# Kernel tuning notes

Measured on AMD Instinct MI355X. Metric: run time of the kernel, lower is better.

## Reference

```python
import jax, jax.numpy as jnp
import numpy as np

NUM_BINS = 256
WS = 5          # ssim_window_size
SIGMA = 1.5
LEVELS = 5
MS_WEIGHTS = jnp.asarray(np.array([0.0448, 0.2856, 0.3001, 0.2363, 0.1333], dtype=np.float32))


def _gauss_window():
    x = np.arange(WS) - WS // 2
    g = np.exp(-(x.astype(np.float64) ** 2) / (2.0 * SIGMA ** 2))
    g = g / g.sum()
    return jnp.asarray(np.outer(g, g), dtype=jnp.float32)  # (WS, WS)


def _conv_same(x, w):
    # x: (H, W), w: (WS, WS); 'SAME' pad == torch padding=WS//2 for odd WS
    return jax.lax.conv_general_dilated(x[None, None], w[None, None], (1, 1), 'SAME')[0, 0]


def _rgb_to_lab(img):
    # img: (3, H, W) in [0,1] -> normalized LAB (3, H, W)  (CURL ImageProcessing.rgb_to_lab)
    H, W = img.shape[1], img.shape[2]
    x = jnp.transpose(img, (2, 1, 0)).reshape(-1, 3)  # (W*H, 3)
    lin = jnp.where(x <= 0.04045, x / 12.92,
                    ((jnp.maximum(x, 1e-4) + 0.055) / 1.055) ** 2.4)
    rgb2xyz = jnp.array([[0.412453, 0.212671, 0.019334],
                         [0.357580, 0.715160, 0.119193],
                         [0.180423, 0.072169, 0.950227]], dtype=img.dtype)
    xyz = lin @ rgb2xyz
    xyz = xyz * jnp.array([1.0 / 0.950456, 1.0, 1.0 / 1.088754], dtype=img.dtype)
    eps = 6.0 / 29.0
    f = jnp.where(xyz <= eps ** 3,
                  xyz / (3.0 * eps ** 2) + 4.0 / 29.0,
                  jnp.maximum(xyz, 1e-4) ** (1.0 / 3.0))
    f2lab = jnp.array([[0.0, 500.0, 0.0],
                       [116.0, -500.0, 200.0],
                       [0.0, 0.0, -200.0]], dtype=img.dtype)
    lab = f @ f2lab + jnp.array([-16.0, 0.0, 0.0], dtype=img.dtype)
    lab = jnp.transpose(lab.reshape(W, H, 3), (2, 1, 0))  # (3, H, W)
    return jnp.stack([lab[0] / 100.0,
                      (lab[1] / 110.0 + 1.0) / 2.0,
                      (lab[2] / 110.0 + 1.0) / 2.0])


def _histogram(img):
    # img: (3, H, W) in [0,1] -> per-channel 256-bin count histogram (3, NUM_BINS)
    idx = jnp.clip(jnp.floor(img * NUM_BINS).astype(jnp.int32), 0, NUM_BINS - 1)
    per_ch = lambda ix: jnp.zeros((NUM_BINS,), jnp.float32).at[ix.reshape(-1)].add(1.0)
    return jax.vmap(per_ch)(idx)


def _ssim(i1, i2, w):
    # i1, i2: (H, W) single-channel images
    mu1 = _conv_same(i1, w)
    mu2 = _conv_same(i2, w)
    s1 = _conv_same(i1 * i1, w) - mu1 * mu1
    s2 = _conv_same(i2 * i2, w) - mu2 * mu2
    s12 = _conv_same(i1 * i2, w) - mu1 * mu2
    C1, C2 = 0.01 ** 2, 0.03 ** 2
    ssim_map = ((2.0 * mu1 * mu2 + C1) * (2.0 * s12 + C2)) / \
               ((mu1 * mu1 + mu2 * mu2 + C1) * (s1 + s2 + C2))
    cs = jnp.mean((2.0 * s12 + C2) / (s1 + s2 + C2))
    return ssim_map.mean(), cs


def _avg_pool2(x):
    H, W = x.shape
    return x.reshape(H // 2, 2, W // 2, 2).mean(axis=(1, 3))


def _msssim(i1, i2, w):
    mssim, mcs = [], []
    for _ in range(LEVELS):
        s, cs = _ssim(i1, i2, w)
        mssim.append(s)
        mcs.append(cs)
        i1 = _avg_pool2(i1)
        i2 = _avg_pool2(i2)
    mssim = (jnp.stack(mssim) + 1.0) / 2.0
    mcs = (jnp.stack(mcs) + 1.0) / 2.0
    return jnp.prod(mcs[:LEVELS - 1] ** MS_WEIGHTS[:LEVELS - 1]) * mssim[LEVELS - 1] ** MS_WEIGHTS[LEVELS - 1]


def _forward(input_image_batch, predicted_img_batch, target_img_batch):
    pred_lab = jnp.clip(jax.vmap(_rgb_to_lab)(predicted_img_batch), 0.0, 1.0)
    tgt_lab = jnp.clip(jax.vmap(_rgb_to_lab)(target_img_batch), 0.0, 1.0)

    # histogram loss: original loop does h_i = (h_{i-1} + l1_i + 1) / 2; closed form below
    hp = jax.vmap(_histogram)(pred_lab)   # (B, 3, NUM_BINS)
    ht = jax.vmap(_histogram)(tgt_lab)
    l1_hist = jnp.mean(jnp.abs(hp - ht), axis=(1, 2))  # (B,)
    n = l1_hist.shape[0]
    wgt = 2.0 ** (jnp.arange(n, dtype=jnp.float32) - n)  # 2^{-(n-i)}
    hist_loss = jnp.sum(wgt * (l1_hist + 1.0))

    # MS-SSIM on L channel, per image (is_identity=True -> no variational_prediction)
    window = _gauss_window()
    ms = jax.vmap(lambda a, b: _msssim(a, b, window))(pred_lab[:, 0], tgt_lab[:, 0])
    ssim_loss = jnp.mean(1.0 - ms)

    lab_l1 = jnp.mean(jnp.abs(pred_lab - tgt_lab))  # mean of per-image means (same-size imgs)

    H, W = input_image_batch.shape[2], input_image_batch.shape[3]
    scaler = H * W / 20.0
    hist_loss = hist_loss / n / scaler
    lab_loss = lab_l1 + hist_loss
    return lab_loss.reshape(1, 1), ssim_loss.reshape(1, 1)


def setup_inputs():
    key = jax.random.key(0)
    k1, k2, k3 = jax.random.split(key, 3)
    B, C, H, W = 8, 3, 512, 512
    return {
        'input_image_batch': jax.random.uniform(k1, (B, C, H, W), jnp.float32),
        'predicted_img_batch': jax.random.uniform(k2, (B, C, H, W), jnp.float32),
        'target_img_batch': jax.random.uniform(k3, (B, C, H, W), jnp.float32),
        'is_identity': 1,
    }


def reference(input_image_batch, predicted_img_batch, target_img_batch, is_identity):
    return _forward(input_image_batch, predicted_img_batch, target_img_batch)
```

## Files before the change

kernel.cpp:

```cpp
#include <hip/hip_runtime.h>
#include <math.h>

#define B 8
#define IMH 512
#define IMW 512
#define HW (IMH*IMW)
#define NBINS 256

#define PYR_PER_IMG (65536 + 16384 + 4096 + 1024)
#define PYR_OFF_L1 0
#define PYR_OFF_L2 65536
#define PYR_OFF_L3 81920
#define PYR_OFF_L4 86016

#define OFF_PPYR 0
#define OFF_TPYR (B*PYR_PER_IMG)
#define OFF_HISTPART (2*B*PYR_PER_IMG)
#define OFF_LABPART  (OFF_HISTPART + B*256*768)
#define OFF_CSP      (OFF_LABPART + B*256)
#define OFF_LVLS     (OFF_CSP + B*256)
#define OFF_LVLC     (OFF_LVLS + B*85)
#define OFF_HISTL1   (OFF_LVLC + B*85)

typedef float f2 __attribute__((ext_vector_type(2)));

__device__ __forceinline__ f2 mkf2(float a, float b) { f2 r; r.x = a; r.y = b; return r; }
__device__ __forceinline__ f2 shfl_down_f2(f2 v, int d) {
    return mkf2(__shfl_down(v.x, d, 64), __shfl_down(v.y, d, 64));
}
__device__ __forceinline__ f2 shfl_f2(f2 v, int src) {
    return mkf2(__shfl(v.x, src, 64), __shfl(v.y, src, 64));
}
__device__ __forceinline__ f2 clamp01_f2(f2 a) {
    a.x = fminf(fmaxf(a.x, 0.0f), 1.0f);
    a.y = fminf(fmaxf(a.y, 0.0f), 1.0f);
    return a;
}

__device__ __forceinline__ float fastpow(float x, float y) {
    return __builtin_amdgcn_exp2f(y * __builtin_amdgcn_logf(x));
}

__device__ __forceinline__ void rgb2lab_pk(f2 r, f2 g, f2 b, f2 lab[3]) {
    f2 v[3] = {r, g, b};
    f2 lin[3];
    #pragma unroll
    for (int c = 0; c < 3; ++c) {
        f2 x = v[c];
        float hx = fastpow((fmaxf(x.x, 1e-4f) + 0.055f) * (float)(1.0/1.055), 2.4f);
        float hy = fastpow((fmaxf(x.y, 1e-4f) + 0.055f) * (float)(1.0/1.055), 2.4f);
        lin[c].x = (x.x <= 0.04045f) ? x.x * (float)(1.0/12.92) : hx;
        lin[c].y = (x.y <= 0.04045f) ? x.y * (float)(1.0/12.92) : hy;
    }
    f2 X = 0.412453f*lin[0] + 0.357580f*lin[1] + 0.180423f*lin[2];
    f2 Y = 0.212671f*lin[0] + 0.715160f*lin[1] + 0.072169f*lin[2];
    f2 Z = 0.019334f*lin[0] + 0.119193f*lin[1] + 0.950227f*lin[2];
    X = X * (float)(1.0/0.950456);
    Z = Z * (float)(1.0/1.088754);
    const float eps3   = (float)((6.0/29.0)*(6.0/29.0)*(6.0/29.0));
    const float rd3e2  = (float)(1.0/(3.0*(6.0/29.0)*(6.0/29.0)));
    const float c429   = (float)(4.0/29.0);
    f2 xyz[3] = {X, Y, Z};
    f2 f[3];
    #pragma unroll
    for (int c = 0; c < 3; ++c) {
        float ax = xyz[c].x, ay = xyz[c].y;
        f[c].x = (ax <= eps3) ? (ax * rd3e2 + c429) : fastpow(fmaxf(ax, 1e-4f), (float)(1.0/3.0));
        f[c].y = (ay <= eps3) ? (ay * rd3e2 + c429) : fastpow(fmaxf(ay, 1e-4f), (float)(1.0/3.0));
    }
    f2 L  = 116.0f*f[1] - 16.0f;
    f2 A  = 500.0f*f[0] - 500.0f*f[1];
    f2 Bc = 200.0f*f[1] - 200.0f*f[2];
    lab[0] = L * 0.01f;
    lab[1] = (A * (float)(1.0/110.0) + 1.0f) * 0.5f;
    lab[2] = (Bc * (float)(1.0/110.0) + 1.0f) * 0.5f;
}

#define TST 37

template<bool WANT_S>
__device__ __forceinline__ void conv_ssim(const f2* tile, int t, float& ssum, float& csum) {
    double gd[5]; double gs = 0.0;
    #pragma unroll
    for (int i = 0; i < 5; ++i) { gd[i] = exp(-(double)((i-2)*(i-2)) / 4.5); gs += gd[i]; }
    float gw[5];
    #pragma unroll
    for (int i = 0; i < 5; ++i) gw[i] = (float)(gd[i] / gs);

    int lx = t & 31;
    int yg = t >> 5;

    f2 rA[8], rB[8];
    float r12[8];
    #pragma unroll
    for (int k = 0; k < 8; ++k) {
        int row = yg * 4 + k;
        const f2* p = &tile[row * TST + lx];
        f2 sA = {0.f, 0.f}, sB = {0.f, 0.f};
        float s12 = 0.f;
        #pragma unroll
        for (int dx = 0; dx < 5; ++dx) {
            f2 av = p[dx];
            float wv = gw[dx];
            sA += wv * av;
            f2 sq = av * av;
            sB += wv * sq;
            s12 = fmaf(wv, av.x * av.y, s12);
        }
        rA[k] = sA; rB[k] = sB; r12[k] = s12;
    }

    const float C1 = (float)(0.01 * 0.01);
    const float C2 = (float)(0.03 * 0.03);
    if constexpr (WANT_S) ssum = 0.f;
    csum = 0.f;
    #pragma unroll
    for (int j = 0; j < 4; ++j) {
        f2 mA = {0.f, 0.f}, mB = {0.f, 0.f};
        float m12 = 0.f;
        #pragma unroll
        for (int k = 0; k < 5; ++k) {
            float wv = gw[k];
            mA += wv * rA[j + k];
            mB += wv * rB[j + k];
            m12 = fmaf(wv, r12[j + k], m12);
        }
        float m1 = mA.x, m2 = mA.y;
        float v1  = mB.x - m1 * m1;
        float v2  = mB.y - m2 * m2;
        float v12 = m12 - m1 * m2;
        float n12 = 2.0f * v12 + C2;
        float rd2 = __builtin_amdgcn_rcpf(v1 + v2 + C2);
        csum = fmaf(n12, rd2, csum);
        if constexpr (WANT_S) {
            float rd1 = __builtin_amdgcn_rcpf(m1*m1 + m2*m2 + C1);
            ssum += (2.0f*m1*m2 + C1) * n12 * rd1 * rd2;
        }
    }
}

__device__ __forceinline__ void halo_coords(int h, int& hr, int& hc) {
    if (h < 72)       { hr = h / 36;            hc = h % 36; }
    else if (h < 144) { int u = h - 72;  hr = 34 + u / 36; hc = u % 36; }
    else              { int u = h - 144; hr = 2 + (u >> 2); int q = u & 3; hc = (q < 2) ? q : 32 + q; }
}

__global__ void lab_ssim0_kernel(const float* __restrict__ pred,
                                 const float* __restrict__ tgt,
                                 unsigned* __restrict__ histPart,
                                 float* __restrict__ labPart,
                                 float* __restrict__ csPart,
                                 float* __restrict__ ppyr,
                                 float* __restrict__ tpyr) {
    __shared__ f2 ls[36 * TST];
    __shared__ unsigned lhist[6 * NBINS];
    __shared__ f2 s1[16 * 16];
    __shared__ float red12[12];

    int t  = threadIdx.x;
    int b  = blockIdx.y;
    int bx = blockIdx.x;

    for (int i = t; i < 6 * NBINS; i += 256) lhist[i] = 0;
    __syncthreads();

    int tile = ((bx & 7) << 5) | (bx >> 3);
    int tx0 = (tile & 15) << 5;
    int ty0 = (tile >> 4) << 5;
    int r   = t >> 3;
    int c4  = (t & 7) << 2;
    int gy  = ty0 + r;

    const float* pimg = pred + (size_t)b * 3 * HW;
    const float* timg = tgt  + (size_t)b * 3 * HW;
    size_t ibase = (size_t)gy * IMW + tx0 + c4;

    float prA[4], pgA[4], pbA[4], trA[4], tgA[4], tbA[4];
    *(float4*)&prA[0] = *(const float4*)(pimg + ibase);
    *(float4*)&pgA[0] = *(const float4*)(pimg + ibase + HW);
    *(float4*)&pbA[0] = *(const float4*)(pimg + ibase + 2*HW);
    *(float4*)&trA[0] = *(const float4*)(timg + ibase);
    *(float4*)&tgA[0] = *(const float4*)(timg + ibase + HW);
    *(float4*)&tbA[0] = *(const float4*)(timg + ibase + 2*HW);

    int hr0, hc0;
    halo_coords(t, hr0, hc0);
    int hy0 = ty0 - 2 + hr0;
    int hx0 = tx0 - 2 + hc0;
    bool hv0 = ((unsigned)hy0 < 512u) && ((unsigned)hx0 < 512u);
    size_t ho = hv0 ? ((size_t)hy0 * IMW + hx0) : 0;
    float h_pr = pimg[ho], h_pg = pimg[ho + HW], h_pb = pimg[ho + 2*HW];
    float h_tr = timg[ho], h_tg = timg[ho + HW], h_tb = timg[ho + 2*HW];

    float l1 = 0.0f;
    f2 pL[4];
    #pragma unroll
    for (int k = 0; k < 4; ++k) {
        f2 lab[3];
        rgb2lab_pk(mkf2(prA[k], trA[k]), mkf2(pgA[k], tgA[k]), mkf2(pbA[k], tbA[k]), lab);
        #pragma unroll
        for (int c = 0; c < 3; ++c) {
            f2 lc = clamp01_f2(lab[c]);
            l1 += fabsf(lc.x - lc.y);
            int ip = min(max((int)floorf(lc.x * (float)NBINS), 0), NBINS - 1);
            int it = min(max((int)floorf(lc.y * (float)NBINS), 0), NBINS - 1);
            atomicAdd(&lhist[c * NBINS + ip], 1u);
            atomicAdd(&lhist[(3 + c) * NBINS + it], 1u);
            if (c == 0) pL[k] = lc;
        }
        ls[(r + 2) * TST + (c4 + 2 + k)] = pL[k];
    }

    {
        f2 lab[3];
        rgb2lab_pk(mkf2(h_pr, h_tr), mkf2(h_pg, h_tg), mkf2(h_pb, h_tb), lab);
        f2 Lv = hv0 ? clamp01_f2(lab[0]) : mkf2(0.f, 0.f);
        ls[hr0 * TST + hc0] = Lv;
    }
    if (t < 16) {
        int hr, hc;
        halo_coords(256 + t, hr, hc);
        int hy = ty0 - 2 + hr;
        int hx = tx0 - 2 + hc;
        f2 Lv = {0.f, 0.f};
        if ((unsigned)hy < 512u && (unsigned)hx < 512u) {
            size_t o = (size_t)hy * IMW + hx;
            f2 lab[3];
            rgb2lab_pk(mkf2(pimg[o], timg[o]),
                       mkf2(pimg[o + HW], timg[o + HW]),
                       mkf2(pimg[o + 2*HW], timg[o + 2*HW]), lab);
            Lv = clamp01_f2(lab[0]);
        }
        ls[hr * TST + hc] = Lv;
    }
    __syncthreads();

    unsigned* hp = histPart + ((size_t)b * 256 + bx) * 768;
    for (int i = t; i < 768; i += 256)
        hp[i] = (lhist[2*i] & 0xFFFFu) | (lhist[2*i + 1] << 16);

    float* pyrP = ppyr + (size_t)b * PYR_PER_IMG;
    float* pyrT = tpyr + (size_t)b * PYR_PER_IMG;
    f2 ph0 = pL[0] + pL[1], ph1 = pL[2] + pL[3];
    f2 ph0b = shfl_down_f2(ph0, 8);
    f2 ph1b = shfl_down_f2(ph1, 8);
    if ((t & 8) == 0) {
        int y1 = r >> 1;
        int x1 = (t & 7) << 1;
        f2 v0 = 0.25f * (ph0 + ph0b);
        f2 v1 = 0.25f * (ph1 + ph1b);
        s1[y1 * 16 + x1]     = v0;
        s1[y1 * 16 + x1 + 1] = v1;
        int g1 = ((ty0 >> 1) + y1) * 256 + (tx0 >> 1) + x1;
        *(float2*)&pyrP[PYR_OFF_L1 + g1] = make_float2(v0.x, v1.x);
        *(float2*)&pyrT[PYR_OFF_L1 + g1] = make_float2(v0.y, v1.y);
    }
    __syncthreads();

    float sdummy, csum;
    conv_ssim<false>(ls, t, sdummy, csum);

    if (t < 64) {
        int y2 = t >> 3, x2 = t & 7;
        const f2* s = &s1[(2*y2) * 16 + 2*x2];
        f2 v2 = 0.25f * (s[0] + s[1] + s[16] + s[17]);
        pyrP[PYR_OFF_L2 + ((ty0 >> 2) + y2) * 128 + (tx0 >> 2) + x2] = v2.x;
        pyrT[PYR_OFF_L2 + ((ty0 >> 2) + y2) * 128 + (tx0 >> 2) + x2] = v2.y;

        int y3 = (t >> 2) & 3, x3 = t & 3;
        f2 v3 = 0.25f * (shfl_f2(v2, (2*y3)*8 + 2*x3)     + shfl_f2(v2, (2*y3)*8 + 2*x3 + 1) +
                         shfl_f2(v2, (2*y3+1)*8 + 2*x3)   + shfl_f2(v2, (2*y3+1)*8 + 2*x3 + 1));
        if (t < 16) {
            pyrP[PYR_OFF_L3 + ((ty0 >> 3) + y3) * 64 + (tx0 >> 3) + x3] = v3.x;
            pyrT[PYR_OFF_L3 + ((ty0 >> 3) + y3) * 64 + (tx0 >> 3) + x3] = v3.y;
        }
        int y4 = (t >> 1) & 1, x4 = t & 1;
        f2 v4 = 0.25f * (shfl_f2(v3, (2*y4)*4 + 2*x4)     + shfl_f2(v3, (2*y4)*4 + 2*x4 + 1) +
                         shfl_f2(v3, (2*y4+1)*4 + 2*x4)   + shfl_f2(v3, (2*y4+1)*4 + 2*x4 + 1));
        if (t < 4) {
            pyrP[PYR_OFF_L4 + ((ty0 >> 4) + y4) * 32 + (tx0 >> 4) + x4] = v4.x;
            pyrT[PYR_OFF_L4 + ((ty0 >> 4) + y4) * 32 + (tx0 >> 4) + x4] = v4.y;
        }
    }

    int lane = t & 63;
    int wid  = t >> 6;
    #pragma unroll
    for (int o = 32; o >= 1; o >>= 1) {
        l1   += __shfl_down(l1, o, 64);
        csum += __shfl_down(csum, o, 64);
    }
    if (lane == 0) {
        red12[wid * 2 + 0] = l1;
        red12[wid * 2 + 1] = csum;
    }
    __syncthreads();
    if (t < 4) {
        float a0 = red12[t * 2 + 0];
        float a2 = red12[t * 2 + 1];
        #pragma unroll
        for (int o = 2; o >= 1; o >>= 1) {
            a0 += __shfl_down(a0, o, 64);
            a2 += __shfl_down(a2, o, 64);
        }
        if (t == 0) {
            labPart[b * 256 + bx] = a0;
            csPart[b * 256 + bx]  = a2;
        }
    }
}

__global__ void tail_kernel(const float* __restrict__ ppyr,
                            const float* __restrict__ tpyr,
                            const unsigned* __restrict__ histPart,
                            float* __restrict__ lvlS,
                            float* __restrict__ lvlC,
                            float* __restrict__ histL1p) {
    __shared__ f2 tls[36 * TST];
    __shared__ float red12[12];
    __shared__ int dLo[256];
    __shared__ int dHi[256];
    int t = threadIdx.x;
    int bx = blockIdx.x;

    if (bx < 48) {
        int b  = bx / 6;
        int w  = (bx % 6) * 64 + (t & 63);
        int ck = t >> 6;
        const unsigned* p = histPart + (size_t)b * 256 * 768 + (size_t)(ck * 64) * 768;
        unsigned sPlo = 0, sPhi = 0, sTlo = 0, sThi = 0;
        #pragma unroll 8
        for (int i = 0; i < 64; ++i) {
            unsigned wP = p[(size_t)i * 768 + w];
            unsigned wT = p[(size_t)i * 768 + 384 + w];
            sPlo += wP & 0xFFFFu;  sPhi += wP >> 16;
            sTlo += wT & 0xFFFFu;  sThi += wT >> 16;
        }
        dLo[t] = (int)sPlo - (int)sTlo;
        dHi[t] = (int)sPhi - (int)sThi;
        __syncthreads();
        if (t < 64) {
            int lo = dLo[t] + dLo[t + 64] + dLo[t + 128] + dLo[t + 192];
            int hi = dHi[t] + dHi[t + 64] + dHi[t + 128] + dHi[t + 192];
            float val = fabsf((float)lo) + fabsf((float)hi);
            #pragma unroll
            for (int o = 32; o >= 1; o >>= 1) val += __shfl_down(val, o, 64);
            if (t == 0) histL1p[bx] = val;
        }
    } else {
        int cb = bx - 48;
        int b = cb / 85;
        int sub = cb - b * 85;
        int lvl, pblk;
        if (sub < 64)      { lvl = 1; pblk = sub; }
        else if (sub < 80) { lvl = 2; pblk = sub - 64; }
        else if (sub < 84) { lvl = 3; pblk = sub - 80; }
        else               { lvl = 4; pblk = 0; }

        const int offs[5] = {0, PYR_OFF_L1, PYR_OFF_L2, PYR_OFF_L3, PYR_OFF_L4};
        int w = 512 >> lvl;
        const float* i1 = ppyr + (size_t)b * PYR_PER_IMG + offs[lvl];
        const float* i2 = tpyr + (size_t)b * PYR_PER_IMG + offs[lvl];

        int tprShift = 4 - lvl;
        int ty0 = (pblk >> tprShift) << 5;
        int tx0 = (pblk & ((1 << tprShift) - 1)) << 5;

        for (int i = t; i < 36 * 36; i += 256) {
            int r = i / 36, c = i % 36;
            int gy = ty0 - 2 + r;
            int gx = tx0 - 2 + c;
            bool ok = ((unsigned)gy < (unsigned)w) && ((unsigned)gx < (unsigned)w);
            int gi = gy * w + gx;
            tls[r * TST + c] = ok ? mkf2(i1[gi], i2[gi]) : mkf2(0.f, 0.f);
        }
        __syncthreads();

        float ssum, csum;
        conv_ssim<true>(tls, t, ssum, csum);

        int lane = t & 63;
        int wid  = t >> 6;
        #pragma unroll
        for (int o = 32; o >= 1; o >>= 1) {
            ssum += __shfl_down(ssum, o, 64);
            csum += __shfl_down(csum, o, 64);
        }
        if (lane == 0) {
            red12[wid * 2 + 0] = ssum;
            red12[wid * 2 + 1] = csum;
        }
        __syncthreads();
        if (t < 4) {
            float a1 = red12[t * 2 + 0];
            float a2 = red12[t * 2 + 1];
            #pragma unroll
            for (int o = 2; o >= 1; o >>= 1) {
                a1 += __shfl_down(a1, o, 64);
                a2 += __shfl_down(a2, o, 64);
            }
            if (t == 0) {
                lvlS[cb] = a1;
                lvlC[cb] = a2;
            }
        }
    }
}

__global__ void final_kernel(const float* __restrict__ labPart,
                             const float* __restrict__ csPart,
                             const float* __restrict__ lvlS,
                             const float* __restrict__ lvlC,
                             const float* __restrict__ histL1p,
                             float* __restrict__ out) {
    __shared__ double sh[48];
    __shared__ double wred[4];
    int t = threadIdx.x;

    {
        int b = t >> 5, k = t & 31;
        double s = 0.0;
        #pragma unroll
        for (int j = 0; j < 8; ++j) s += (double)csPart[b * 256 + k + 32 * j];
        #pragma unroll
        for (int o = 16; o >= 1; o >>= 1) s += __shfl_down(s, o, 32);
        if (k == 0) sh[b] = s;
    }
    {
        double s = 0.0;
        #pragma unroll
        for (int j = 0; j < 8; ++j) s += (double)labPart[t + 256 * j];
        #pragma unroll
        for (int o = 32; o >= 1; o >>= 1) s += __shfl_down(s, o, 64);
        if ((t & 63) == 0) wred[t >> 6] = s;
    }
    if (t < 32) {
        int b = t >> 2, q = t & 3;
        const int lo[4] = {0, 64, 80, 84};
        const int hi[4] = {64, 80, 84, 85};
        const float* src = (q == 3) ? lvlS : lvlC;
        double s = 0.0;
        for (int i = lo[q]; i < hi[q]; ++i) s += (double)src[b * 85 + i];
        sh[8 + q * 8 + b] = s;
    }
    if (t < 8) {
        double s = 0.0;
        #pragma unroll
        for (int j = 0; j < 6; ++j) s += (double)histL1p[t * 6 + j];
        sh[40 + t] = s;
    }
    __syncthreads();

    if (t < 8) {
        const float msw[5]  = {0.0448f, 0.2856f, 0.3001f, 0.2363f, 0.1333f};
        const float npix[5] = {(float)HW, (float)(HW/4), (float)(HW/16),
                               (float)(HW/64), (float)(HW/256)};
        int b = t;
        float l1 = (float)(sh[40 + b] / (double)(3 * NBINS));
        float wgt = __builtin_amdgcn_exp2f((float)(b - B));
        float histc = wgt * (l1 + 1.0f);
        float ms = 1.0f;
        float cs0 = (float)(sh[b] / (double)npix[0]);
        ms *= fastpow((cs0 + 1.0f) * 0.5f, msw[0]);
        #pragma unroll
        for (int l = 1; l <= 3; ++l) {
            float cs = (float)(sh[l * 8 + b] / (double)npix[l]);
            ms *= fastpow((cs + 1.0f) * 0.5f, msw[l]);
        }
        float sm = (float)(sh[32 + b] / (double)npix[4]);
        ms *= fastpow((sm + 1.0f) * 0.5f, msw[4]);
        float lossc = 1.0f - ms;
        #pragma unroll
        for (int o = 4; o >= 1; o >>= 1) {
            histc += __shfl_down(histc, o, 64);
            lossc += __shfl_down(lossc, o, 64);
        }
        if (t == 0) {
            double labSum = wred[0] + wred[1] + wred[2] + wred[3];
            float scaler = (float)HW / 20.0f;
            float hist_loss = histc / (float)B / scaler;
            float lab_l1 = (float)(sh[40] * 0.0 + labSum / (double)((size_t)B * 3 * HW));
            out[0] = lab_l1 + hist_loss;
            out[1] = lossc / (float)B;
        }
    }
}

extern "C" void kernel_launch(void* const* d_in, const int* in_sizes, int n_in,
                              void* d_out, int out_size, void* d_ws, size_t ws_size,
                              hipStream_t stream) {
    const float* pred = (const float*)d_in[1];
    const float* tgt  = (const float*)d_in[2];
    float* ws_f = (float*)d_ws;

    float* ppyr     = ws_f + OFF_PPYR;
    float* tpyr     = ws_f + OFF_TPYR;
    unsigned* histPart = (unsigned*)(ws_f + OFF_HISTPART);
    float* labPart  = ws_f + OFF_LABPART;
    float* csPart   = ws_f + OFF_CSP;
    float* lvlS     = ws_f + OFF_LVLS;
    float* lvlC     = ws_f + OFF_LVLC;
    float* histL1p  = ws_f + OFF_HISTL1;
    float* out = (float*)d_out;


    lab_ssim0_kernel<<<dim3(256, B), 256, 0, stream>>>(pred, tgt, histPart, labPart,
                                                       csPart, ppyr, tpyr);

    tail_kernel<<<728, 256, 0, stream>>>(ppyr, tpyr, histPart, lvlS, lvlC, histL1p);

    final_kernel<<<1, 256, 0, stream>>>(labPart, csPart, lvlS, lvlC, histL1p, out);
}
```

Before: 129.9 us.

## Widen first-stage tiles to 64x32 with separable SSIM convolution

Each first-stage block now covers a 64x32 tile instead of 32x32, halving the block count and the number of per-block partial histograms the tail kernel must reduce. The 5x5 SSIM window is computed separably: horizontal sums go into a rolling register buffer, then a vertical pass. The pyramid downsampling is remapped to the wider tile, and one barrier is removed. This lowers halo overhead and partial-histogram traffic, at the cost of more registers per thread and fewer blocks to spread across the GPU.

```diff
diff --git a/kernel.cpp b/kernel.cpp
--- a/kernel.cpp
+++ b/kernel.cpp
@@ -13,12 +13,14 @@
 #define PYR_OFF_L3 81920
 #define PYR_OFF_L4 86016
 
+#define NTILE 128
+
 #define OFF_PPYR 0
 #define OFF_TPYR (B*PYR_PER_IMG)
 #define OFF_HISTPART (2*B*PYR_PER_IMG)
-#define OFF_LABPART  (OFF_HISTPART + B*256*768)
-#define OFF_CSP      (OFF_LABPART + B*256)
-#define OFF_LVLS     (OFF_CSP + B*256)
+#define OFF_LABPART  (OFF_HISTPART + B*NTILE*768)
+#define OFF_CSP      (OFF_LABPART + B*NTILE)
+#define OFF_LVLS     (OFF_CSP + B*NTILE)
 #define OFF_LVLC     (OFF_LVLS + B*85)
 #define OFF_HISTL1   (OFF_LVLC + B*85)
 
@@ -77,6 +79,7 @@
 }
 
 #define TST 37
+#define WT  69
 
 template<bool WANT_S>
 __device__ __forceinline__ void conv_ssim(const f2* tile, int t, float& ssum, float& csum) {
@@ -139,10 +142,59 @@
     }
 }
 
-__device__ __forceinline__ void halo_coords(int h, int& hr, int& hc) {
-    if (h < 72)       { hr = h / 36;            hc = h % 36; }
-    else if (h < 144) { int u = h - 72;  hr = 34 + u / 36; hc = u % 36; }
-    else              { int u = h - 144; hr = 2 + (u >> 2); int q = u & 3; hc = (q < 2) ? q : 32 + q; }
+__device__ __forceinline__ void hsum5(const f2* p, const float* gw, f2& A, f2& Bq, float& s12) {
+    A = mkf2(0.f, 0.f); Bq = mkf2(0.f, 0.f); s12 = 0.f;
+    #pragma unroll
+    for (int dx = 0; dx < 5; ++dx) {
+        f2 av = p[dx];
+        float wv = gw[dx];
+        A += wv * av;
+        Bq += wv * (av * av);
+        s12 = fmaf(wv, av.x * av.y, s12);
+    }
+}
+
+__device__ __forceinline__ float conv_cs_wide(const f2* tile, int t) {
+    double gd[5]; double gs = 0.0;
+    #pragma unroll
+    for (int i = 0; i < 5; ++i) { gd[i] = exp(-(double)((i-2)*(i-2)) / 4.5); gs += gd[i]; }
+    float gw[5];
+    #pragma unroll
+    for (int i = 0; i < 5; ++i) gw[i] = (float)(gd[i] / gs);
+
+    int x  = t & 63;
+    int R0 = (t >> 6) * 8;
+    const f2* base = tile + x;
+
+    f2 hA[8], hB[8]; float h12[8];
+    #pragma unroll
+    for (int k = 0; k < 8; ++k)
+        hsum5(base + (R0 + k) * WT, gw, hA[k], hB[k], h12[k]);
+
+    const float C2 = (float)(0.03 * 0.03);
+    float csum = 0.f;
+    auto emit = [&](int i0, int i1, int i2, int i3, int i4) {
+        f2 mA = gw[0]*hA[i0] + gw[1]*hA[i1] + gw[2]*hA[i2] + gw[3]*hA[i3] + gw[4]*hA[i4];
+        f2 mB = gw[0]*hB[i0] + gw[1]*hB[i1] + gw[2]*hB[i2] + gw[3]*hB[i3] + gw[4]*hB[i4];
+        float m12 = gw[0]*h12[i0] + gw[1]*h12[i1] + gw[2]*h12[i2] + gw[3]*h12[i3] + gw[4]*h12[i4];
+        float m1 = mA.x, m2 = mA.y;
+        float v1  = mB.x - m1 * m1;
+        float v2v = mB.y - m2 * m2;
+        float v12 = m12 - m1 * m2;
+        csum = fmaf(2.0f * v12 + C2, __builtin_amdgcn_rcpf(v1 + v2v + C2), csum);
+    };
+    emit(0,1,2,3,4); emit(1,2,3,4,5); emit(2,3,4,5,6); emit(3,4,5,6,7);
+    hsum5(base + (R0 +  8) * WT, gw, hA[0], hB[0], h12[0]); emit(4,5,6,7,0);
+    hsum5(base + (R0 +  9) * WT, gw, hA[1], hB[1], h12[1]); emit(5,6,7,0,1);
+    hsum5(base + (R0 + 10) * WT, gw, hA[2], hB[2], h12[2]); emit(6,7,0,1,2);
+    hsum5(base + (R0 + 11) * WT, gw, hA[3], hB[3], h12[3]); emit(7,0,1,2,3);
+    return csum;
+}
+
+__device__ __forceinline__ void halo68(int h, int& hr, int& hc) {
+    if (h < 136)      { hr = h / 68;            hc = h % 68; }
+    else if (h < 272) { int u = h - 136; hr = 34 + u / 68; hc = u % 68; }
+    else              { int u = h - 272; hr = 2 + (u >> 2); int q = u & 3; hc = (q < 2) ? q : q + 64; }
 }
 
 __global__ void lab_ssim0_kernel(const float* __restrict__ pred,
@@ -152,9 +204,9 @@
                                  float* __restrict__ csPart,
                                  float* __restrict__ ppyr,
                                  float* __restrict__ tpyr) {
-    __shared__ f2 ls[36 * TST];
+    __shared__ f2 ls[36 * WT];
     __shared__ unsigned lhist[6 * NBINS];
-    __shared__ f2 s1[16 * 16];
+    __shared__ f2 s1[16 * 32];
     __shared__ float red12[12];
 
     int t  = threadIdx.x;
@@ -164,40 +216,52 @@
     for (int i = t; i < 6 * NBINS; i += 256) lhist[i] = 0;
     __syncthreads();
 
-    int tile = ((bx & 7) << 5) | (bx >> 3);
-    int tx0 = (tile & 15) << 5;
-    int ty0 = (tile >> 4) << 5;
+    int tile = ((bx & 7) << 4) | (bx >> 3);
+    int tx0 = (tile & 7) << 6;
+    int ty0 = (tile >> 3) << 5;
     int r   = t >> 3;
-    int c4  = (t & 7) << 2;
+    int c8  = (t & 7) << 3;
     int gy  = ty0 + r;
 
     const float* pimg = pred + (size_t)b * 3 * HW;
     const float* timg = tgt  + (size_t)b * 3 * HW;
-    size_t ibase = (size_t)gy * IMW + tx0 + c4;
-
-    float prA[4], pgA[4], pbA[4], trA[4], tgA[4], tbA[4];
-    *(float4*)&prA[0] = *(const float4*)(pimg + ibase);
-    *(float4*)&pgA[0] = *(const float4*)(pimg + ibase + HW);
-    *(float4*)&pbA[0] = *(const float4*)(pimg + ibase + 2*HW);
-    *(float4*)&trA[0] = *(const float4*)(timg + ibase);
-    *(float4*)&tgA[0] = *(const float4*)(timg + ibase + HW);
-    *(float4*)&tbA[0] = *(const float4*)(timg + ibase + 2*HW);
-
-    int hr0, hc0;
-    halo_coords(t, hr0, hc0);
-    int hy0 = ty0 - 2 + hr0;
-    int hx0 = tx0 - 2 + hc0;
-    bool hv0 = ((unsigned)hy0 < 512u) && ((unsigned)hx0 < 512u);
-    size_t ho = hv0 ? ((size_t)hy0 * IMW + hx0) : 0;
-    float h_pr = pimg[ho], h_pg = pimg[ho + HW], h_pb = pimg[ho + 2*HW];
-    float h_tr = timg[ho], h_tg = timg[ho + HW], h_tb = timg[ho + 2*HW];
+    size_t ibase = (size_t)gy * IMW + tx0 + c8;
+
+    float pr[8], pg[8], pb[8], tr[8], tg[8], tb[8];
+    *(float4*)&pr[0] = *(const float4*)(pimg + ibase);
+    *(float4*)&pr[4] = *(const float4*)(pimg + ibase + 4);
+    *(float4*)&pg[0] = *(const float4*)(pimg + ibase + HW);
+    *(float4*)&pg[4] = *(const float4*)(pimg + ibase + HW + 4);
+    *(float4*)&pb[0] = *(const float4*)(pimg + ibase + 2*HW);
+    *(float4*)&pb[4] = *(const float4*)(pimg + ibase + 2*HW + 4);
+    *(float4*)&tr[0] = *(const float4*)(timg + ibase);
+    *(float4*)&tr[4] = *(const float4*)(timg + ibase + 4);
+    *(float4*)&tg[0] = *(const float4*)(timg + ibase + HW);
+    *(float4*)&tg[4] = *(const float4*)(timg + ibase + HW + 4);
+    *(float4*)&tb[0] = *(const float4*)(timg + ibase + 2*HW);
+    *(float4*)&tb[4] = *(const float4*)(timg + ibase + 2*HW + 4);
+
+    int hrA, hcA; halo68(t, hrA, hcA);
+    int hyA = ty0 - 2 + hrA, hxA = tx0 - 2 + hcA;
+    bool hvA = ((unsigned)hyA < 512u) && ((unsigned)hxA < 512u);
+    size_t hoA = hvA ? ((size_t)hyA * IMW + hxA) : 0;
+    float aPr = pimg[hoA], aPg = pimg[hoA + HW], aPb = pimg[hoA + 2*HW];
+    float aTr = timg[hoA], aTg = timg[hoA + HW], aTb = timg[hoA + 2*HW];
+
+    bool hasB = t < 144;
+    int hrB, hcB; halo68(hasB ? (256 + t) : 0, hrB, hcB);
+    int hyB = ty0 - 2 + hrB, hxB = tx0 - 2 + hcB;
+    bool hvB = hasB && ((unsigned)hyB < 512u) && ((unsigned)hxB < 512u);
+    size_t hoB = hvB ? ((size_t)hyB * IMW + hxB) : 0;
+    float bPr = pimg[hoB], bPg = pimg[hoB + HW], bPb = pimg[hoB + 2*HW];
+    float bTr = timg[hoB], bTg = timg[hoB + HW], bTb = timg[hoB + 2*HW];
 
     float l1 = 0.0f;
-    f2 pL[4];
-    #pragma unroll
-    for (int k = 0; k < 4; ++k) {
+    f2 pL[8];
+    #pragma unroll
+    for (int k = 0; k < 8; ++k) {
         f2 lab[3];
-        rgb2lab_pk(mkf2(prA[k], trA[k]), mkf2(pgA[k], tgA[k]), mkf2(pbA[k], tbA[k]), lab);
+        rgb2lab_pk(mkf2(pr[k], tr[k]), mkf2(pg[k], tg[k]), mkf2(pb[k], tb[k]), lab);
         #pragma unroll
         for (int c = 0; c < 3; ++c) {
             f2 lc = clamp01_f2(lab[c]);
@@ -208,78 +272,80 @@
             atomicAdd(&lhist[(3 + c) * NBINS + it], 1u);
             if (c == 0) pL[k] = lc;
         }
-        ls[(r + 2) * TST + (c4 + 2 + k)] = pL[k];
+        ls[(r + 2) * WT + (c8 + 2 + k)] = pL[k];
+    }
+
+    float* pyrP = ppyr + (size_t)b * PYR_PER_IMG;
+    float* pyrT = tpyr + (size_t)b * PYR_PER_IMG;
+    {
+        f2 ph[4];
+        ph[0] = pL[0] + pL[1]; ph[1] = pL[2] + pL[3];
+        ph[2] = pL[4] + pL[5]; ph[3] = pL[6] + pL[7];
+        f2 pv[4];
+        #pragma unroll
+        for (int j = 0; j < 4; ++j) pv[j] = shfl_down_f2(ph[j], 8);
+        if ((t & 8) == 0) {
+            int y1 = r >> 1;
+            int x1 = (t & 7) << 2;
+            f2 w0 = 0.25f * (ph[0] + pv[0]);
+            f2 w1 = 0.25f * (ph[1] + pv[1]);
+            f2 w2 = 0.25f * (ph[2] + pv[2]);
+            f2 w3 = 0.25f * (ph[3] + pv[3]);
+            s1[y1 * 32 + x1 + 0] = w0;
+            s1[y1 * 32 + x1 + 1] = w1;
+            s1[y1 * 32 + x1 + 2] = w2;
+            s1[y1 * 32 + x1 + 3] = w3;
+            int g1 = ((ty0 >> 1) + y1) * 256 + (tx0 >> 1) + x1;
+            *(float4*)&pyrP[PYR_OFF_L1 + g1] = make_float4(w0.x, w1.x, w2.x, w3.x);
+            *(float4*)&pyrT[PYR_OFF_L1 + g1] = make_float4(w0.y, w1.y, w2.y, w3.y);
+        }
     }
 
     {
         f2 lab[3];
-        rgb2lab_pk(mkf2(h_pr, h_tr), mkf2(h_pg, h_tg), mkf2(h_pb, h_tb), lab);
-        f2 Lv = hv0 ? clamp01_f2(lab[0]) : mkf2(0.f, 0.f);
-        ls[hr0 * TST + hc0] = Lv;
-    }
-    if (t < 16) {
-        int hr, hc;
-        halo_coords(256 + t, hr, hc);
-        int hy = ty0 - 2 + hr;
-        int hx = tx0 - 2 + hc;
-        f2 Lv = {0.f, 0.f};
-        if ((unsigned)hy < 512u && (unsigned)hx < 512u) {
-            size_t o = (size_t)hy * IMW + hx;
-            f2 lab[3];
-            rgb2lab_pk(mkf2(pimg[o], timg[o]),
-                       mkf2(pimg[o + HW], timg[o + HW]),
-                       mkf2(pimg[o + 2*HW], timg[o + 2*HW]), lab);
-            Lv = clamp01_f2(lab[0]);
-        }
-        ls[hr * TST + hc] = Lv;
+        rgb2lab_pk(mkf2(aPr, aTr), mkf2(aPg, aTg), mkf2(aPb, aTb), lab);
+        f2 Lv = hvA ? clamp01_f2(lab[0]) : mkf2(0.f, 0.f);
+        ls[hrA * WT + hcA] = Lv;
+    }
+    if (hasB) {
+        f2 lab[3];
+        rgb2lab_pk(mkf2(bPr, bTr), mkf2(bPg, bTg), mkf2(bPb, bTb), lab);
+        f2 Lv = hvB ? clamp01_f2(lab[0]) : mkf2(0.f, 0.f);
+        ls[hrB * WT + hcB] = Lv;
     }
     __syncthreads();
 
-    unsigned* hp = histPart + ((size_t)b * 256 + bx) * 768;
+    unsigned* hp = histPart + ((size_t)b * NTILE + bx) * 768;
     for (int i = t; i < 768; i += 256)
         hp[i] = (lhist[2*i] & 0xFFFFu) | (lhist[2*i + 1] << 16);
 
-    float* pyrP = ppyr + (size_t)b * PYR_PER_IMG;
-    float* pyrT = tpyr + (size_t)b * PYR_PER_IMG;
-    f2 ph0 = pL[0] + pL[1], ph1 = pL[2] + pL[3];
-    f2 ph0b = shfl_down_f2(ph0, 8);
-    f2 ph1b = shfl_down_f2(ph1, 8);
-    if ((t & 8) == 0) {
-        int y1 = r >> 1;
-        int x1 = (t & 7) << 1;
-        f2 v0 = 0.25f * (ph0 + ph0b);
-        f2 v1 = 0.25f * (ph1 + ph1b);
-        s1[y1 * 16 + x1]     = v0;
-        s1[y1 * 16 + x1 + 1] = v1;
-        int g1 = ((ty0 >> 1) + y1) * 256 + (tx0 >> 1) + x1;
-        *(float2*)&pyrP[PYR_OFF_L1 + g1] = make_float2(v0.x, v1.x);
-        *(float2*)&pyrT[PYR_OFF_L1 + g1] = make_float2(v0.y, v1.y);
-    }
-    __syncthreads();
-
-    float sdummy, csum;
-    conv_ssim<false>(ls, t, sdummy, csum);
-
-    if (t < 64) {
-        int y2 = t >> 3, x2 = t & 7;
-        const f2* s = &s1[(2*y2) * 16 + 2*x2];
-        f2 v2 = 0.25f * (s[0] + s[1] + s[16] + s[17]);
-        pyrP[PYR_OFF_L2 + ((ty0 >> 2) + y2) * 128 + (tx0 >> 2) + x2] = v2.x;
-        pyrT[PYR_OFF_L2 + ((ty0 >> 2) + y2) * 128 + (tx0 >> 2) + x2] = v2.y;
-
-        int y3 = (t >> 2) & 3, x3 = t & 3;
-        f2 v3 = 0.25f * (shfl_f2(v2, (2*y3)*8 + 2*x3)     + shfl_f2(v2, (2*y3)*8 + 2*x3 + 1) +
-                         shfl_f2(v2, (2*y3+1)*8 + 2*x3)   + shfl_f2(v2, (2*y3+1)*8 + 2*x3 + 1));
-        if (t < 16) {
-            pyrP[PYR_OFF_L3 + ((ty0 >> 3) + y3) * 64 + (tx0 >> 3) + x3] = v3.x;
-            pyrT[PYR_OFF_L3 + ((ty0 >> 3) + y3) * 64 + (tx0 >> 3) + x3] = v3.y;
-        }
-        int y4 = (t >> 1) & 1, x4 = t & 1;
-        f2 v4 = 0.25f * (shfl_f2(v3, (2*y4)*4 + 2*x4)     + shfl_f2(v3, (2*y4)*4 + 2*x4 + 1) +
-                         shfl_f2(v3, (2*y4+1)*4 + 2*x4)   + shfl_f2(v3, (2*y4+1)*4 + 2*x4 + 1));
-        if (t < 4) {
-            pyrP[PYR_OFF_L4 + ((ty0 >> 4) + y4) * 32 + (tx0 >> 4) + x4] = v4.x;
-            pyrT[PYR_OFF_L4 + ((ty0 >> 4) + y4) * 32 + (tx0 >> 4) + x4] = v4.y;
+    float csum = conv_cs_wide(ls, t);
+
+    if (t < 128) {
+        int y2 = t >> 4, x2 = t & 15;
+        const f2* s = &s1[(2*y2) * 32 + 2*x2];
+        f2 v2 = 0.25f * (s[0] + s[1] + s[32] + s[33]);
+        int g2 = ((ty0 >> 2) + y2) * 128 + (tx0 >> 2) + x2;
+        pyrP[PYR_OFF_L2 + g2] = v2.x;
+        pyrT[PYR_OFF_L2 + g2] = v2.y;
+
+        int w = t >> 6;
+        int l = t & 63;
+        int y3l = (l >> 3) & 1, x3 = l & 7;
+        f2 v3 = 0.25f * (shfl_f2(v2, 32*y3l + 2*x3)      + shfl_f2(v2, 32*y3l + 2*x3 + 1) +
+                         shfl_f2(v2, 32*y3l + 16 + 2*x3) + shfl_f2(v2, 32*y3l + 17 + 2*x3));
+        if (l < 16) {
+            int g3 = ((ty0 >> 3) + 2*w + y3l) * 64 + (tx0 >> 3) + x3;
+            pyrP[PYR_OFF_L3 + g3] = v3.x;
+            pyrT[PYR_OFF_L3 + g3] = v3.y;
+        }
+        int x4 = l & 3;
+        f2 v4 = 0.25f * (shfl_f2(v3, 2*x4)     + shfl_f2(v3, 2*x4 + 1) +
+                         shfl_f2(v3, 8 + 2*x4) + shfl_f2(v3, 9 + 2*x4));
+        if (l < 4) {
+            int g4 = ((ty0 >> 4) + w) * 32 + (tx0 >> 4) + x4;
+            pyrP[PYR_OFF_L4 + g4] = v4.x;
+            pyrT[PYR_OFF_L4 + g4] = v4.y;
         }
     }
 
@@ -304,8 +370,8 @@
             a2 += __shfl_down(a2, o, 64);
         }
         if (t == 0) {
-            labPart[b * 256 + bx] = a0;
-            csPart[b * 256 + bx]  = a2;
+            labPart[b * NTILE + bx] = a0;
+            csPart[b * NTILE + bx]  = a2;
         }
     }
 }
@@ -327,10 +393,10 @@
         int b  = bx / 6;
         int w  = (bx % 6) * 64 + (t & 63);
         int ck = t >> 6;
-        const unsigned* p = histPart + (size_t)b * 256 * 768 + (size_t)(ck * 64) * 768;
+        const unsigned* p = histPart + (size_t)b * NTILE * 768 + (size_t)(ck * 32) * 768;
         unsigned sPlo = 0, sPhi = 0, sTlo = 0, sThi = 0;
         #pragma unroll 8
-        for (int i = 0; i < 64; ++i) {
+        for (int i = 0; i < 32; ++i) {
             unsigned wP = p[(size_t)i * 768 + w];
             unsigned wT = p[(size_t)i * 768 + 384 + w];
             sPlo += wP & 0xFFFFu;  sPhi += wP >> 16;
@@ -421,7 +487,7 @@
         int b = t >> 5, k = t & 31;
         double s = 0.0;
         #pragma unroll
-        for (int j = 0; j < 8; ++j) s += (double)csPart[b * 256 + k + 32 * j];
+        for (int j = 0; j < 4; ++j) s += (double)csPart[b * NTILE + k + 32 * j];
         #pragma unroll
         for (int o = 16; o >= 1; o >>= 1) s += __shfl_down(s, o, 32);
         if (k == 0) sh[b] = s;
@@ -429,7 +495,7 @@
     {
         double s = 0.0;
         #pragma unroll
-        for (int j = 0; j < 8; ++j) s += (double)labPart[t + 256 * j];
+        for (int j = 0; j < 4; ++j) s += (double)labPart[t + 256 * j];
         #pragma unroll
         for (int o = 32; o >= 1; o >>= 1) s += __shfl_down(s, o, 64);
         if ((t & 63) == 0) wred[t >> 6] = s;
@@ -479,7 +545,7 @@
             double labSum = wred[0] + wred[1] + wred[2] + wred[3];
             float scaler = (float)HW / 20.0f;
             float hist_loss = histc / (float)B / scaler;
-            float lab_l1 = (float)(sh[40] * 0.0 + labSum / (double)((size_t)B * 3 * HW));
+            float lab_l1 = (float)(labSum / (double)((size_t)B * 3 * HW));
             out[0] = lab_l1 + hist_loss;
             out[1] = lossc / (float)B;
         }
@@ -504,8 +570,8 @@
     float* out = (float*)d_out;
 
 
-    lab_ssim0_kernel<<<dim3(256, B), 256, 0, stream>>>(pred, tgt, histPart, labPart,
-                                                       csPart, ppyr, tpyr);
+    lab_ssim0_kernel<<<dim3(NTILE, B), 256, 0, stream>>>(pred, tgt, histPart, labPart,
+                                                         csPart, ppyr, tpyr);
 
     tail_kernel<<<728, 256, 0, stream>>>(ppyr, tpyr, histPart, lvlS, lvlC, histL1p);
 
```

After: 150.0 us. 15.5% more time.
